# Kernel tuning notes

Hardware: AMD Instinct MI355X
Metric: run time of the kernel (lower is better)

The kernel has to match this reference:

```python
import jax, jax.numpy as jnp
import numpy as np

GRID_N = 8
N_RAYS = 4096
CHUNK = 512
MAX_SAMPLES = 128
SAMPLING_LENGTH = 0.05
STEP = SAMPLING_LENGTH / MAX_SAMPLES
HIT_THRESH = 5.0


def _build_mesh(n):
    g = n + 1
    xs = np.linspace(0.0, 1.0, g)
    P = np.stack(np.meshgrid(xs, xs, xs, indexing='ij'), -1).reshape(-1, 3).astype(np.float32)

    def vid(i, j, k):
        return (i * g + j) * g + k

    perms = [(0, 1, 2), (0, 2, 1), (1, 0, 2), (1, 2, 0), (2, 0, 1), (2, 1, 0)]
    tets = []
    for i in range(n):
        for j in range(n):
            for k in range(n):
                base = np.array([i, j, k])
                for p in perms:
                    vlist = [base.copy()]
                    cur = base.copy()
                    for ax in p:
                        cur = cur.copy(); cur[ax] += 1
                        vlist.append(cur.copy())
                    tets.append([vid(*vv) for vv in vlist])
    tets = np.array(tets, dtype=np.int32)  # [T,4]
    A, B, C, D = tets.T
    # face order matches torch module: ABC, ABD, ACD, BCD
    faces = np.stack([np.stack([A, B, C], 1), np.stack([A, B, D], 1),
                      np.stack([A, C, D], 1), np.stack([B, C, D], 1)], 1).astype(np.int32)  # [T,4,3]
    ff = faces.reshape(-1, 3)
    sf = np.sort(ff, 1)
    order = np.lexsort((sf[:, 2], sf[:, 1], sf[:, 0]))
    ss = sf[order]
    eq = np.all(ss[:-1] == ss[1:], 1)
    topo = -np.ones((tets.shape[0], 4), dtype=np.int32)
    idx = np.where(eq)[0]
    a = order[idx]; b = order[idx + 1]
    topo[a // 4, a % 4] = b // 4
    topo[b // 4, b % 4] = a // 4
    return P, tets, faces, topo


def setup_inputs() -> dict:
    key = jax.random.key(0)
    k1, k2, k3 = jax.random.split(key, 3)
    P, tets, faces, topo = _build_mesh(GRID_N)
    cage = jnp.asarray(P)[None] + 0.005 * jax.random.normal(k1, (1, P.shape[0], 3), jnp.float32)
    xy = jax.random.uniform(k2, (N_RAYS, 2), jnp.float32, 0.15, 0.85)
    ro = jnp.concatenate([xy, jnp.full((N_RAYS, 1), -0.5, jnp.float32)], -1)[None]
    jit = 0.05 * jax.random.normal(k3, (N_RAYS, 2), jnp.float32)
    rd = jnp.concatenate([jit, jnp.ones((N_RAYS, 1), jnp.float32)], -1)
    rd = (rd / jnp.linalg.norm(rd, axis=-1, keepdims=True))[None]
    return {"cage_vertices": cage, "ro": ro, "rd": rd,
            "tetras": jnp.asarray(tets), "faces": jnp.asarray(faces),
            "topology": jnp.asarray(topo)}


def _intersect(tri, o, d):
    # Moller-Trumbore: tri [F,3,3], o/d [c,3] -> nearest hit t + face idx
    p0 = tri[:, 0]; e1 = tri[:, 1] - p0; e2 = tri[:, 2] - p0
    h = jnp.cross(d[:, None, :], e2[None])          # [c,F,3]
    a = jnp.sum(e1[None] * h, -1)                   # [c,F]
    f = 1.0 / jnp.where(jnp.abs(a) > 1e-9, a, 1e-9)
    s = o[:, None, :] - p0[None]
    u = f * jnp.sum(s * h, -1)
    q = jnp.cross(s, e1[None])
    v = f * jnp.sum(d[:, None, :] * q, -1)
    t = f * jnp.sum(e2[None] * q, -1)
    ok = (jnp.abs(a) > 1e-9) & (u >= 0) & (u <= 1) & (v >= 0) & (u + v <= 1) & (t > 1e-6)
    t = jnp.where(ok, t, 1e10)
    return jnp.min(t, 1), jnp.argmin(t, 1)


def _bary(verts, tetras, p, tet):
    # barycentric coords of p [R,3] inside tetra tet [R] -> [R,4]
    vv = verts[tetras[tet]]                                # [R,4,3]
    M = jnp.transpose(vv[:, 1:] - vv[:, :1], (0, 2, 1))    # [R,3,3] columns B-A,C-A,D-A
    w = jnp.linalg.solve(M, (p - vv[:, 0])[..., None])[..., 0]  # wB,wC,wD
    return jnp.concatenate([1.0 - jnp.sum(w, -1, keepdims=True), w], -1)


def reference(cage_vertices, ro, rd, tetras, faces, topology):
    verts = cage_vertices[0]                 # [V,3]
    tri = verts[faces.reshape(-1, 3)]        # [F,3,3] deformed tetra faces
    o = ro[0]; d = rd[0]
    R = o.shape[0]
    od = jnp.concatenate([o, d], -1).reshape(R // CHUNK, CHUNK, 6)
    tmin, fidx = jax.lax.map(lambda x: _intersect(tri, x[:, :3], x[:, 3:]), od)
    tmin = tmin.reshape(R); fidx = fidx.reshape(R)
    hit = tmin < HIT_THRESH                  # mask = distances < 5
    t0 = jnp.where(hit, tmin, 0.0)
    hitp = o + t0[:, None] * d               # closest_points
    tet0 = jnp.where(hit, (fidx // 4).astype(jnp.int32), 0)  # triangle_to_tetra

    def step(carry, k):
        tet, alive = carry
        p = hitp + (k.astype(jnp.float32) * STEP + 1e-4) * d
        for _ in range(3):  # up to 3 neighbor hops per sample (tetra walk)
            w = _bary(verts, tetras, p, tet)
            inside = jnp.all(w >= -1e-6, -1)
            nb = topology[tet, 3 - jnp.argmin(w, -1)]  # face opposite most-negative vert
            move = alive & ~inside
            tet = jnp.where(move & (nb >= 0), nb, tet)
            alive = alive & (inside | (nb >= 0))
        w = _bary(verts, tetras, p, tet)
        inside = jnp.all(w >= -1e-6, -1)
        valid = alive & inside
        m = valid[:, None].astype(w.dtype)
        return (tet, alive), (jnp.where(valid, tet, -1), w * m, p * m, valid)

    (_, _), (tet_s, w_s, p_s, valid_s) = jax.lax.scan(step, (tet0, hit), jnp.arange(MAX_SAMPLES))
    tetra_indices = jnp.transpose(tet_s)            # [R,S]
    bary_coords = jnp.transpose(w_s, (1, 0, 2))     # [R,S,4]
    deformed_positions = jnp.transpose(p_s, (1, 0, 2))  # [R,S,3]
    valid = jnp.transpose(valid_s)
    ray_indices = jnp.where(valid, jnp.arange(R, dtype=jnp.int32)[:, None], -1)
    t_start = t0
    t_end = jnp.where(hit, t0 + SAMPLING_LENGTH, 0.0)
    return ray_indices, tetra_indices, bary_coords, t_start, t_end, deformed_positions
```

## Files before the change

kernel.cpp:

```cpp
#include <hip/hip_runtime.h>

#define S_MAX 128
#define NV_MAX 729
#define STEPD (0.05 / 128.0)
#define GUARD 1e-12

static __device__ __forceinline__ double mt_eval_f64(
    int F, const int* __restrict__ faces,
    const float* sx, const float* sy, const float* sz,
    double ox, double oy, double oz,
    double dx, double dy, double dz)
{
    const int i0 = faces[3 * F + 0];
    const int i1 = faces[3 * F + 1];
    const int i2 = faces[3 * F + 2];
    const double p0x = (double)sx[i0], p0y = (double)sy[i0], p0z = (double)sz[i0];
    const double e1x = (double)sx[i1] - p0x, e1y = (double)sy[i1] - p0y, e1z = (double)sz[i1] - p0z;
    const double e2x = (double)sx[i2] - p0x, e2y = (double)sy[i2] - p0y, e2z = (double)sz[i2] - p0z;
    const double hx = dy * e2z - dz * e2y;
    const double hy = dz * e2x - dx * e2z;
    const double hz = dx * e2y - dy * e2x;
    const double a  = e1x * hx + e1y * hy + e1z * hz;
    const bool oka = fabs(a) > 1e-9;
    const double f  = 1.0 / (oka ? a : 1e-9);
    const double s0 = ox - p0x, s1 = oy - p0y, s2 = oz - p0z;
    const double u  = f * (s0 * hx + s1 * hy + s2 * hz);
    const double qx = s1 * e1z - s2 * e1y;
    const double qy = s2 * e1x - s0 * e1z;
    const double qz = s0 * e1y - s1 * e1x;
    const double v  = f * (dx * qx + dy * qy + dz * qz);
    double t        = f * (e2x * qx + e2y * qy + e2z * qz);
    const bool ok = oka && (u >= 0.0) && (u <= 1.0) && (v >= 0.0) &&
                    (u + v <= 1.0) && (t > 1e-6);
    return ok ? t : 1e10;
}

__global__ __launch_bounds__(256) void isect_prep_kernel(
    const float* __restrict__ verts,
    const float* __restrict__ ro,
    const float* __restrict__ rd,
    const int*   __restrict__ faces,
    const int*   __restrict__ tetras,
    double* __restrict__ winv,
    double* __restrict__ tmin_out,
    int*    __restrict__ fidx_out,
    int NV, int NT, int NF, int R, int nIsect)
{
    const int tid = threadIdx.x;

    if (blockIdx.x >= nIsect) {
        const int t = (blockIdx.x - nIsect) * 256 + tid;
        if (t < NT) {
            const int4 tv = ((const int4*)tetras)[t];
            const double v0x = (double)verts[3 * tv.x + 0];
            const double v0y = (double)verts[3 * tv.x + 1];
            const double v0z = (double)verts[3 * tv.x + 2];
            const double m11 = (double)verts[3 * tv.y + 0] - v0x, m21 = (double)verts[3 * tv.y + 1] - v0y, m31 = (double)verts[3 * tv.y + 2] - v0z;
            const double m12 = (double)verts[3 * tv.z + 0] - v0x, m22 = (double)verts[3 * tv.z + 1] - v0y, m32 = (double)verts[3 * tv.z + 2] - v0z;
            const double m13 = (double)verts[3 * tv.w + 0] - v0x, m23 = (double)verts[3 * tv.w + 1] - v0y, m33 = (double)verts[3 * tv.w + 2] - v0z;
            const double A = m22 * m33 - m23 * m32;
            const double B = m21 * m33 - m23 * m31;
            const double C = m21 * m32 - m22 * m31;
            const double det = m11 * A - m12 * B + m13 * C;
            const double rcp = 1.0 / det;
            double* o = winv + 12 * (size_t)t;
            o[0] = v0x; o[1] = v0y; o[2] = v0z;
            o[3]  = A * rcp;  o[4]  = (m13 * m32 - m12 * m33) * rcp;  o[5]  = (m12 * m23 - m13 * m22) * rcp;
            o[6]  = -B * rcp; o[7]  = (m11 * m33 - m13 * m31) * rcp;  o[8]  = (m13 * m21 - m11 * m23) * rcp;
            o[9]  = C * rcp;  o[10] = (m12 * m31 - m11 * m32) * rcp;  o[11] = (m11 * m22 - m12 * m21) * rcp;
        }
        return;
    }

    __shared__ float sx[NV_MAX], sy[NV_MAX], sz[NV_MAX];
    __shared__ float red[256];
    __shared__ float s_zmin, s_zmax, s_marg;

    for (int i = tid; i < NV; i += 256) {
        sx[i] = verts[3 * i + 0];
        sy[i] = verts[3 * i + 1];
        sz[i] = verts[3 * i + 2];
    }
    __syncthreads();

    float zmin = 1e9f, zmax = -1e9f, dev = 0.0f;
    for (int i = tid; i < NV; i += 256) {
        const float x = sx[i], y = sy[i], z = sz[i];
        if (i % 9 == 0) { zmin = fminf(zmin, z); zmax = fmaxf(zmax, z); }
        dev = fmaxf(dev, fabsf(x - rintf(x * 8.0f) * 0.125f));
        dev = fmaxf(dev, fabsf(y - rintf(y * 8.0f) * 0.125f));
    }
    red[tid] = zmin; __syncthreads();
    for (int s = 128; s; s >>= 1) { if (tid < s) red[tid] = fminf(red[tid], red[tid + s]); __syncthreads(); }
    if (tid == 0) s_zmin = red[0];
    __syncthreads();
    red[tid] = zmax; __syncthreads();
    for (int s = 128; s; s >>= 1) { if (tid < s) red[tid] = fmaxf(red[tid], red[tid + s]); __syncthreads(); }
    if (tid == 0) s_zmax = red[0];
    __syncthreads();
    red[tid] = dev; __syncthreads();
    for (int s = 128; s; s >>= 1) { if (tid < s) red[tid] = fmaxf(red[tid], red[tid + s]); __syncthreads(); }
    if (tid == 0) s_marg = red[0] + 1e-5f;
    __syncthreads();

    const int wv = tid >> 6, lane = tid & 63;
    const int r = blockIdx.x * 4 + wv;
    if (r >= R) return;

    const double ox = (double)ro[3 * r + 0], oy = (double)ro[3 * r + 1], oz = (double)ro[3 * r + 2];
    const double dx = (double)rd[3 * r + 0], dy = (double)rd[3 * r + 1], dz = (double)rd[3 * r + 2];

    int ncand = 0, ixlo = 0, iylo = 0, ny = 1;
    if (dz > 0.0) {
        const double t_lo = ((double)s_zmin - oz) / dz;
        const double t_hi = ((double)s_zmax - oz) / dz;
        const double marg = (double)s_marg + 1e-9;
        const double xa = ox + t_lo * dx, xb = ox + t_hi * dx;
        const double ya = oy + t_lo * dy, yb = oy + t_hi * dy;
        const double xlo = fmin(xa, xb) - marg, xhi = fmax(xa, xb) + marg;
        const double ylo = fmin(ya, yb) - marg, yhi = fmax(ya, yb) + marg;
        const int ix0 = max(0, (int)floor(xlo * 8.0)), ix1 = min(7, (int)floor(xhi * 8.0));
        const int iy0 = max(0, (int)floor(ylo * 8.0)), iy1 = min(7, (int)floor(yhi * 8.0));
        if (ix0 <= ix1 && iy0 <= iy1) {
            ixlo = ix0; iylo = iy0;
            ny = iy1 - iy0 + 1;
            ncand = (ix1 - ix0 + 1) * ny * 24;
        }
    }

    double bt = 1e10;
    int    bi = 0x7fffffff;
    for (int c = lane; c < ncand; c += 64) {
        const int cell = c / 24, fk = c - cell * 24;
        const int cx = cell / ny, cy = cell - cx * ny;
        const int F = ((ixlo + cx) * 64 + (iylo + cy) * 8) * 24 + fk;
        const double t = mt_eval_f64(F, faces, sx, sy, sz, ox, oy, oz, dx, dy, dz);
        if (t < bt || (t == bt && F < bi)) { bt = t; bi = F; }
    }
    for (int off = 32; off; off >>= 1) {
        const double t2 = __shfl_down(bt, off);
        const int    i2 = __shfl_down(bi, off);
        if (t2 < bt || (t2 == bt && i2 < bi)) { bt = t2; bi = i2; }
    }
    const double btw = __shfl(bt, 0);
    if (btw >= 1e10) {
        bt = 1e10; bi = 0x7fffffff;
        for (int F = lane; F < NF; F += 64) {
            const double t = mt_eval_f64(F, faces, sx, sy, sz, ox, oy, oz, dx, dy, dz);
            if (t < bt || (t == bt && F < bi)) { bt = t; bi = F; }
        }
        for (int off = 32; off; off >>= 1) {
            const double t2 = __shfl_down(bt, off);
            const int    i2 = __shfl_down(bi, off);
            if (t2 < bt || (t2 == bt && i2 < bi)) { bt = t2; bi = i2; }
        }
    }
    if (lane == 0) { tmin_out[r] = bt; fidx_out[r] = bi; }
}

__global__ __launch_bounds__(256) void walk_kernel(
    const float* __restrict__ ro,
    const float* __restrict__ rd,
    const int*   __restrict__ topo,
    const double* __restrict__ tmin_in,
    const int*    __restrict__ fidx_in,
    const double* __restrict__ winv,
    short* __restrict__ seq,
    float* __restrict__ out_tstart,
    float* __restrict__ out_tend,
    int R)
{
    const int wv = threadIdx.x >> 6, lane = threadIdx.x & 63;
    const int r = blockIdx.x * 4 + wv;
    if (r >= R) return;

    short* myseq = seq + (size_t)r * S_MAX;

    const double tmin = tmin_in[r];
    const bool   hit  = tmin < 5.0;
    const double t0   = hit ? tmin : 0.0;
    if (lane == 0) {
        out_tstart[r] = (float)t0;
        out_tend[r]   = hit ? (float)(t0 + 0.05) : 0.0f;
    }
    if (!hit) {
        for (int k = lane; k < S_MAX; k += 64) myseq[k] = -1;
        return;
    }

    const double ox = (double)ro[3 * r + 0], oy = (double)ro[3 * r + 1], oz = (double)ro[3 * r + 2];
    const double dx = (double)rd[3 * r + 0], dy = (double)rd[3 * r + 1], dz = (double)rd[3 * r + 2];
    const double hpx = ox + t0 * dx, hpy = oy + t0 * dy, hpz = oz + t0 * dz;

    int  tet   = fidx_in[r] >> 2;
    bool alive = true;

    int4 topo4 = ((const int4*)topo)[tet];
    const double* rec = winv + 12 * (size_t)tet;
    double v0x = rec[0], v0y = rec[1], v0z = rec[2];
    double i0 = rec[3], i1 = rec[4],  i2 = rec[5];
    double i3 = rec[6], i4 = rec[7],  i5 = rec[8];
    double i6 = rec[9], i7 = rec[10], i8 = rec[11];

    double wb0, wb1, wb2, wb3, wd0, wd1, wd2, wd3;
    {
        const double bx = hpx - v0x, by = hpy - v0y, bz = hpz - v0z;
        wb1 = i0 * bx + i1 * by + i2 * bz;
        wb2 = i3 * bx + i4 * by + i5 * bz;
        wb3 = i6 * bx + i7 * by + i8 * bz;
        wd1 = i0 * dx + i1 * dy + i2 * dz;
        wd2 = i3 * dx + i4 * dy + i5 * dz;
        wd3 = i6 * dx + i7 * dy + i8 * dz;
        wb0 = 1.0 - (wb1 + wb2 + wb3);
        wd0 = -(wd1 + wd2 + wd3);
    }

    int k0 = 0;
    while (k0 < S_MAX) {
        const int kk = k0 + lane;
        bool p = false;
        if (kk < S_MAX) {
            const double toff = (double)kk * STEPD + 1e-4;
            const double a0 = wb0 + toff * wd0;
            const double a1 = wb1 + toff * wd1;
            const double a2 = wb2 + toff * wd2;
            const double a3 = wb3 + toff * wd3;
            const double mn = fmin(fmin(a0, a1), fmin(a2, a3));
            p = (mn + 1e-6 >= GUARD);
        }
        const unsigned long long bad = __ballot(kk < S_MAX && !p);
        const int nvalid = min(S_MAX - k0, 64);
        const int evt = (bad == 0ull) ? nvalid : (__ffsll(bad) - 1);

        if (lane < evt) myseq[kk] = (short)tet;
        k0 += evt;
        if (evt == nvalid) continue;

        const double toff = (double)k0 * STEPD + 1e-4;
        const double px = hpx + toff * dx;
        const double py = hpy + toff * dy;
        const double pz = hpz + toff * dz;

        double b1 = px - v0x, b2 = py - v0y, b3 = pz - v0z;
        double w1 = i0 * b1 + i1 * b2 + i2 * b3;
        double w2 = i3 * b1 + i4 * b2 + i5 * b3;
        double w3 = i6 * b1 + i7 * b2 + i8 * b3;
        double w0 = 1.0 - (w1 + w2 + w3);
        bool inside = (w0 >= -1e-6) && (w1 >= -1e-6) && (w2 >= -1e-6) && (w3 >= -1e-6);

        int it = 0;
        bool moved = false;
        while (!inside && it < 3) {
            int    jm = 0;
            double wb = w0;
            if (w1 < wb) { wb = w1; jm = 1; }
            if (w2 < wb) { wb = w2; jm = 2; }
            if (w3 < wb) { wb = w3; jm = 3; }
            const int nb = (jm == 0) ? topo4.w : (jm == 1) ? topo4.z :
                           (jm == 2) ? topo4.y : topo4.x;
            if (nb < 0) { alive = false; break; }
            tet = nb;
            moved = true;
            rec = winv + 12 * (size_t)tet;
            topo4 = ((const int4*)topo)[tet];
            v0x = rec[0]; v0y = rec[1]; v0z = rec[2];
            i0 = rec[3]; i1 = rec[4];  i2 = rec[5];
            i3 = rec[6]; i4 = rec[7];  i5 = rec[8];
            i6 = rec[9]; i7 = rec[10]; i8 = rec[11];
            b1 = px - v0x; b2 = py - v0y; b3 = pz - v0z;
            w1 = i0 * b1 + i1 * b2 + i2 * b3;
            w2 = i3 * b1 + i4 * b2 + i5 * b3;
            w3 = i6 * b1 + i7 * b2 + i8 * b3;
            w0 = 1.0 - (w1 + w2 + w3);
            inside = (w0 >= -1e-6) && (w1 >= -1e-6) && (w2 >= -1e-6) && (w3 >= -1e-6);
            ++it;
        }
        if (!alive) break;

        if (lane == 0) myseq[k0] = inside ? (short)tet : (short)-1;
        ++k0;

        if (moved) {
            const double bx = hpx - v0x, by = hpy - v0y, bz = hpz - v0z;
            wb1 = i0 * bx + i1 * by + i2 * bz;
            wb2 = i3 * bx + i4 * by + i5 * bz;
            wb3 = i6 * bx + i7 * by + i8 * bz;
            wd1 = i0 * dx + i1 * dy + i2 * dz;
            wd2 = i3 * dx + i4 * dy + i5 * dz;
            wd3 = i6 * dx + i7 * dy + i8 * dz;
            wb0 = 1.0 - (wb1 + wb2 + wb3);
            wd0 = -(wd1 + wd2 + wd3);
        }
    }
    for (int k = k0 + lane; k < S_MAX; k += 64) myseq[k] = -1;
}

__global__ __launch_bounds__(256) void emit_kernel(
    const float* __restrict__ ro,
    const float* __restrict__ rd,
    const double* __restrict__ tmin_in,
    const short*  __restrict__ seq,
    const double* __restrict__ winv,
    float* __restrict__ out_rayidx,
    float* __restrict__ out_tetidx,
    float* __restrict__ out_bary,
    float* __restrict__ out_pos,
    int R)
{
    const int idx = blockIdx.x * 256 + threadIdx.x;
    if (idx >= R * S_MAX) return;
    const int r = idx >> 7;
    const int k = idx & (S_MAX - 1);

    const int tk = (int)seq[idx];
    if (tk < 0) {
        out_rayidx[idx] = -1.0f;
        out_tetidx[idx] = -1.0f;
        ((float4*)out_bary)[idx] = make_float4(0.0f, 0.0f, 0.0f, 0.0f);
        out_pos[idx * 3 + 0] = 0.0f;
        out_pos[idx * 3 + 1] = 0.0f;
        out_pos[idx * 3 + 2] = 0.0f;
        return;
    }

    const double tmin = tmin_in[r];
    const double t0   = (tmin < 5.0) ? tmin : 0.0;
    const double ox = (double)ro[3 * r + 0], oy = (double)ro[3 * r + 1], oz = (double)ro[3 * r + 2];
    const double dx = (double)rd[3 * r + 0], dy = (double)rd[3 * r + 1], dz = (double)rd[3 * r + 2];
    const double toff = (double)k * STEPD + 1e-4;
    const double px = (ox + t0 * dx) + toff * dx;
    const double py = (oy + t0 * dy) + toff * dy;
    const double pz = (oz + t0 * dz) + toff * dz;

    const double* rec = winv + 12 * (size_t)tk;
    const double b1 = px - rec[0], b2 = py - rec[1], b3 = pz - rec[2];
    const double w1 = rec[3] * b1 + rec[4]  * b2 + rec[5]  * b3;
    const double w2 = rec[6] * b1 + rec[7]  * b2 + rec[8]  * b3;
    const double w3 = rec[9] * b1 + rec[10] * b2 + rec[11] * b3;
    const double w0 = 1.0 - (w1 + w2 + w3);

    out_rayidx[idx] = (float)r;
    out_tetidx[idx] = (float)tk;
    ((float4*)out_bary)[idx] = make_float4((float)w0, (float)w1, (float)w2, (float)w3);
    out_pos[idx * 3 + 0] = (float)px;
    out_pos[idx * 3 + 1] = (float)py;
    out_pos[idx * 3 + 2] = (float)pz;
}

extern "C" void kernel_launch(void* const* d_in, const int* in_sizes, int n_in,
                              void* d_out, int out_size, void* d_ws, size_t ws_size,
                              hipStream_t stream) {
    const float* verts  = (const float*)d_in[0];
    const float* ro     = (const float*)d_in[1];
    const float* rd     = (const float*)d_in[2];
    const int*   tetras = (const int*)d_in[3];
    const int*   faces  = (const int*)d_in[4];
    const int*   topo   = (const int*)d_in[5];

    const int NV = in_sizes[0] / 3;
    const int R  = in_sizes[1] / 3;
    const int NT = in_sizes[3] / 4;
    const int NF = in_sizes[4] / 3;
    const int S  = S_MAX;

    double* wtmin = (double*)d_ws;
    double* winv  = wtmin + R;
    int*    wfidx = (int*)(winv + 12 * (size_t)NT);
    short*  wseq  = (short*)(wfidx + R);

    float* out        = (float*)d_out;
    float* out_rayidx = out;
    float* out_tetidx = out + (size_t)R * S;
    float* out_bary   = out + (size_t)2 * R * S;
    float* out_tstart = out + (size_t)6 * R * S;
    float* out_tend   = out_tstart + R;
    float* out_pos    = out_tend + R;

    const int nIsect = (R + 3) / 4;
    const int nPrep  = (NT + 255) / 256;

    isect_prep_kernel<<<nIsect + nPrep, 256, 0, stream>>>(
        verts, ro, rd, faces, tetras, winv, wtmin, wfidx, NV, NT, NF, R, nIsect);
    walk_kernel<<<(R + 3) / 4, 256, 0, stream>>>(ro, rd, topo, wtmin, wfidx, winv,
                                                 wseq, out_tstart, out_tend, R);
    emit_kernel<<<(R * S + 255) / 256, 256, 0, stream>>>(ro, rd, wtmin, wseq, winv,
                                                         out_rayidx, out_tetidx, out_bary, out_pos, R);
}
```

Measured before the change: 87.50 us.

## Fuse intersection, tetra walk and emit into one per-ray kernel

Moves tetra inverse-matrix prep into its own kernel and merges ray intersection, the tetra walk and output emission into a single kernel. Each wave keeps its ray's tet sequence in shared memory. This drops the global round trips for tmin, face index and the short sequence buffer, and removes one kernel launch. The cost is that emit work now runs 64 lanes per ray instead of using a fully parallel grid, and the prep kernel no longer overlaps with intersection blocks.

```diff
diff --git a/kernel.cpp b/kernel.cpp
--- a/kernel.cpp
+++ b/kernel.cpp
@@ -35,47 +35,54 @@
     return ok ? t : 1e10;
 }
 
-__global__ __launch_bounds__(256) void isect_prep_kernel(
+__global__ __launch_bounds__(256) void prep_kernel(
+    const float* __restrict__ verts,
+    const int*   __restrict__ tetras,
+    double* __restrict__ winv,
+    int NT)
+{
+    const int t = blockIdx.x * 256 + threadIdx.x;
+    if (t >= NT) return;
+    const int4 tv = ((const int4*)tetras)[t];
+    const double v0x = (double)verts[3 * tv.x + 0];
+    const double v0y = (double)verts[3 * tv.x + 1];
+    const double v0z = (double)verts[3 * tv.x + 2];
+    const double m11 = (double)verts[3 * tv.y + 0] - v0x, m21 = (double)verts[3 * tv.y + 1] - v0y, m31 = (double)verts[3 * tv.y + 2] - v0z;
+    const double m12 = (double)verts[3 * tv.z + 0] - v0x, m22 = (double)verts[3 * tv.z + 1] - v0y, m32 = (double)verts[3 * tv.z + 2] - v0z;
+    const double m13 = (double)verts[3 * tv.w + 0] - v0x, m23 = (double)verts[3 * tv.w + 1] - v0y, m33 = (double)verts[3 * tv.w + 2] - v0z;
+    const double A = m22 * m33 - m23 * m32;
+    const double B = m21 * m33 - m23 * m31;
+    const double C = m21 * m32 - m22 * m31;
+    const double det = m11 * A - m12 * B + m13 * C;
+    const double rcp = 1.0 / det;
+    double* o = winv + 12 * (size_t)t;
+    o[0] = v0x; o[1] = v0y; o[2] = v0z;
+    o[3]  = A * rcp;  o[4]  = (m13 * m32 - m12 * m33) * rcp;  o[5]  = (m12 * m23 - m13 * m22) * rcp;
+    o[6]  = -B * rcp; o[7]  = (m11 * m33 - m13 * m31) * rcp;  o[8]  = (m13 * m21 - m11 * m23) * rcp;
+    o[9]  = C * rcp;  o[10] = (m12 * m31 - m11 * m32) * rcp;  o[11] = (m11 * m22 - m12 * m21) * rcp;
+}
+
+__global__ __launch_bounds__(256) void fused_kernel(
     const float* __restrict__ verts,
     const float* __restrict__ ro,
     const float* __restrict__ rd,
     const int*   __restrict__ faces,
-    const int*   __restrict__ tetras,
-    double* __restrict__ winv,
-    double* __restrict__ tmin_out,
-    int*    __restrict__ fidx_out,
-    int NV, int NT, int NF, int R, int nIsect)
+    const int*   __restrict__ topo,
+    const double* __restrict__ winv,
+    float* __restrict__ out_rayidx,
+    float* __restrict__ out_tetidx,
+    float* __restrict__ out_bary,
+    float* __restrict__ out_tstart,
+    float* __restrict__ out_tend,
+    float* __restrict__ out_pos,
+    int NV, int NF, int R)
 {
-    const int tid = threadIdx.x;
-
-    if (blockIdx.x >= nIsect) {
-        const int t = (blockIdx.x - nIsect) * 256 + tid;
-        if (t < NT) {
-            const int4 tv = ((const int4*)tetras)[t];
-            const double v0x = (double)verts[3 * tv.x + 0];
-            const double v0y = (double)verts[3 * tv.x + 1];
-            const double v0z = (double)verts[3 * tv.x + 2];
-            const double m11 = (double)verts[3 * tv.y + 0] - v0x, m21 = (double)verts[3 * tv.y + 1] - v0y, m31 = (double)verts[3 * tv.y + 2] - v0z;
-            const double m12 = (double)verts[3 * tv.z + 0] - v0x, m22 = (double)verts[3 * tv.z + 1] - v0y, m32 = (double)verts[3 * tv.z + 2] - v0z;
-            const double m13 = (double)verts[3 * tv.w + 0] - v0x, m23 = (double)verts[3 * tv.w + 1] - v0y, m33 = (double)verts[3 * tv.w + 2] - v0z;
-            const double A = m22 * m33 - m23 * m32;
-            const double B = m21 * m33 - m23 * m31;
-            const double C = m21 * m32 - m22 * m31;
-            const double det = m11 * A - m12 * B + m13 * C;
-            const double rcp = 1.0 / det;
-            double* o = winv + 12 * (size_t)t;
-            o[0] = v0x; o[1] = v0y; o[2] = v0z;
-            o[3]  = A * rcp;  o[4]  = (m13 * m32 - m12 * m33) * rcp;  o[5]  = (m12 * m23 - m13 * m22) * rcp;
-            o[6]  = -B * rcp; o[7]  = (m11 * m33 - m13 * m31) * rcp;  o[8]  = (m13 * m21 - m11 * m23) * rcp;
-            o[9]  = C * rcp;  o[10] = (m12 * m31 - m11 * m32) * rcp;  o[11] = (m11 * m22 - m12 * m21) * rcp;
-        }
-        return;
-    }
-
     __shared__ float sx[NV_MAX], sy[NV_MAX], sz[NV_MAX];
     __shared__ float red[256];
     __shared__ float s_zmin, s_zmax, s_marg;
-
+    __shared__ short s_seq[4][S_MAX];
+
+    const int tid = threadIdx.x;
     for (int i = tid; i < NV; i += 256) {
         sx[i] = verts[3 * i + 0];
         sy[i] = verts[3 * i + 1];
@@ -106,6 +113,7 @@
     const int wv = tid >> 6, lane = tid & 63;
     const int r = blockIdx.x * 4 + wv;
     if (r >= R) return;
+    short* myseq = s_seq[wv];
 
     const double ox = (double)ro[3 * r + 0], oy = (double)ro[3 * r + 1], oz = (double)ro[3 * r + 2];
     const double dx = (double)rd[3 * r + 0], dy = (double)rd[3 * r + 1], dz = (double)rd[3 * r + 2];
@@ -142,145 +150,47 @@
         const int    i2 = __shfl_down(bi, off);
         if (t2 < bt || (t2 == bt && i2 < bi)) { bt = t2; bi = i2; }
     }
-    const double btw = __shfl(bt, 0);
-    if (btw >= 1e10) {
-        bt = 1e10; bi = 0x7fffffff;
+    bt = __shfl(bt, 0);
+    bi = __shfl(bi, 0);
+    if (bt >= 1e10) {
+        double fb = 1e10; int fi = 0x7fffffff;
         for (int F = lane; F < NF; F += 64) {
             const double t = mt_eval_f64(F, faces, sx, sy, sz, ox, oy, oz, dx, dy, dz);
-            if (t < bt || (t == bt && F < bi)) { bt = t; bi = F; }
+            if (t < fb || (t == fb && F < fi)) { fb = t; fi = F; }
         }
         for (int off = 32; off; off >>= 1) {
-            const double t2 = __shfl_down(bt, off);
-            const int    i2 = __shfl_down(bi, off);
-            if (t2 < bt || (t2 == bt && i2 < bi)) { bt = t2; bi = i2; }
-        }
-    }
-    if (lane == 0) { tmin_out[r] = bt; fidx_out[r] = bi; }
-}
-
-__global__ __launch_bounds__(256) void walk_kernel(
-    const float* __restrict__ ro,
-    const float* __restrict__ rd,
-    const int*   __restrict__ topo,
-    const double* __restrict__ tmin_in,
-    const int*    __restrict__ fidx_in,
-    const double* __restrict__ winv,
-    short* __restrict__ seq,
-    float* __restrict__ out_tstart,
-    float* __restrict__ out_tend,
-    int R)
-{
-    const int wv = threadIdx.x >> 6, lane = threadIdx.x & 63;
-    const int r = blockIdx.x * 4 + wv;
-    if (r >= R) return;
-
-    short* myseq = seq + (size_t)r * S_MAX;
-
-    const double tmin = tmin_in[r];
-    const bool   hit  = tmin < 5.0;
-    const double t0   = hit ? tmin : 0.0;
+            const double t2 = __shfl_down(fb, off);
+            const int    i2 = __shfl_down(fi, off);
+            if (t2 < fb || (t2 == fb && i2 < fi)) { fb = t2; fi = i2; }
+        }
+        bt = __shfl(fb, 0);
+        bi = __shfl(fi, 0);
+    }
+
+    const bool   hit = bt < 5.0;
+    const double t0  = hit ? bt : 0.0;
     if (lane == 0) {
         out_tstart[r] = (float)t0;
         out_tend[r]   = hit ? (float)(t0 + 0.05) : 0.0f;
     }
+
+    const double hpx = ox + t0 * dx, hpy = oy + t0 * dy, hpz = oz + t0 * dz;
+
     if (!hit) {
         for (int k = lane; k < S_MAX; k += 64) myseq[k] = -1;
-        return;
-    }
-
-    const double ox = (double)ro[3 * r + 0], oy = (double)ro[3 * r + 1], oz = (double)ro[3 * r + 2];
-    const double dx = (double)rd[3 * r + 0], dy = (double)rd[3 * r + 1], dz = (double)rd[3 * r + 2];
-    const double hpx = ox + t0 * dx, hpy = oy + t0 * dy, hpz = oz + t0 * dz;
-
-    int  tet   = fidx_in[r] >> 2;
-    bool alive = true;
-
-    int4 topo4 = ((const int4*)topo)[tet];
-    const double* rec = winv + 12 * (size_t)tet;
-    double v0x = rec[0], v0y = rec[1], v0z = rec[2];
-    double i0 = rec[3], i1 = rec[4],  i2 = rec[5];
-    double i3 = rec[6], i4 = rec[7],  i5 = rec[8];
-    double i6 = rec[9], i7 = rec[10], i8 = rec[11];
-
-    double wb0, wb1, wb2, wb3, wd0, wd1, wd2, wd3;
-    {
-        const double bx = hpx - v0x, by = hpy - v0y, bz = hpz - v0z;
-        wb1 = i0 * bx + i1 * by + i2 * bz;
-        wb2 = i3 * bx + i4 * by + i5 * bz;
-        wb3 = i6 * bx + i7 * by + i8 * bz;
-        wd1 = i0 * dx + i1 * dy + i2 * dz;
-        wd2 = i3 * dx + i4 * dy + i5 * dz;
-        wd3 = i6 * dx + i7 * dy + i8 * dz;
-        wb0 = 1.0 - (wb1 + wb2 + wb3);
-        wd0 = -(wd1 + wd2 + wd3);
-    }
-
-    int k0 = 0;
-    while (k0 < S_MAX) {
-        const int kk = k0 + lane;
-        bool p = false;
-        if (kk < S_MAX) {
-            const double toff = (double)kk * STEPD + 1e-4;
-            const double a0 = wb0 + toff * wd0;
-            const double a1 = wb1 + toff * wd1;
-            const double a2 = wb2 + toff * wd2;
-            const double a3 = wb3 + toff * wd3;
-            const double mn = fmin(fmin(a0, a1), fmin(a2, a3));
-            p = (mn + 1e-6 >= GUARD);
-        }
-        const unsigned long long bad = __ballot(kk < S_MAX && !p);
-        const int nvalid = min(S_MAX - k0, 64);
-        const int evt = (bad == 0ull) ? nvalid : (__ffsll(bad) - 1);
-
-        if (lane < evt) myseq[kk] = (short)tet;
-        k0 += evt;
-        if (evt == nvalid) continue;
-
-        const double toff = (double)k0 * STEPD + 1e-4;
-        const double px = hpx + toff * dx;
-        const double py = hpy + toff * dy;
-        const double pz = hpz + toff * dz;
-
-        double b1 = px - v0x, b2 = py - v0y, b3 = pz - v0z;
-        double w1 = i0 * b1 + i1 * b2 + i2 * b3;
-        double w2 = i3 * b1 + i4 * b2 + i5 * b3;
-        double w3 = i6 * b1 + i7 * b2 + i8 * b3;
-        double w0 = 1.0 - (w1 + w2 + w3);
-        bool inside = (w0 >= -1e-6) && (w1 >= -1e-6) && (w2 >= -1e-6) && (w3 >= -1e-6);
-
-        int it = 0;
-        bool moved = false;
-        while (!inside && it < 3) {
-            int    jm = 0;
-            double wb = w0;
-            if (w1 < wb) { wb = w1; jm = 1; }
-            if (w2 < wb) { wb = w2; jm = 2; }
-            if (w3 < wb) { wb = w3; jm = 3; }
-            const int nb = (jm == 0) ? topo4.w : (jm == 1) ? topo4.z :
-                           (jm == 2) ? topo4.y : topo4.x;
-            if (nb < 0) { alive = false; break; }
-            tet = nb;
-            moved = true;
-            rec = winv + 12 * (size_t)tet;
-            topo4 = ((const int4*)topo)[tet];
-            v0x = rec[0]; v0y = rec[1]; v0z = rec[2];
-            i0 = rec[3]; i1 = rec[4];  i2 = rec[5];
-            i3 = rec[6]; i4 = rec[7];  i5 = rec[8];
-            i6 = rec[9]; i7 = rec[10]; i8 = rec[11];
-            b1 = px - v0x; b2 = py - v0y; b3 = pz - v0z;
-            w1 = i0 * b1 + i1 * b2 + i2 * b3;
-            w2 = i3 * b1 + i4 * b2 + i5 * b3;
-            w3 = i6 * b1 + i7 * b2 + i8 * b3;
-            w0 = 1.0 - (w1 + w2 + w3);
-            inside = (w0 >= -1e-6) && (w1 >= -1e-6) && (w2 >= -1e-6) && (w3 >= -1e-6);
-            ++it;
-        }
-        if (!alive) break;
-
-        if (lane == 0) myseq[k0] = inside ? (short)tet : (short)-1;
-        ++k0;
-
-        if (moved) {
+    } else {
+        int  tet   = bi >> 2;
+        bool alive = true;
+
+        int4 topo4 = ((const int4*)topo)[tet];
+        const double* rec = winv + 12 * (size_t)tet;
+        double v0x = rec[0], v0y = rec[1], v0z = rec[2];
+        double i0 = rec[3], i1 = rec[4],  i2 = rec[5];
+        double i3 = rec[6], i4 = rec[7],  i5 = rec[8];
+        double i6 = rec[9], i7 = rec[10], i8 = rec[11];
+
+        double wb0, wb1, wb2, wb3, wd0, wd1, wd2, wd3;
+        {
             const double bx = hpx - v0x, by = hpy - v0y, bz = hpz - v0z;
             wb1 = i0 * bx + i1 * by + i2 * bz;
             wb2 = i3 * bx + i4 * by + i5 * bz;
@@ -291,60 +201,118 @@
             wb0 = 1.0 - (wb1 + wb2 + wb3);
             wd0 = -(wd1 + wd2 + wd3);
         }
-    }
-    for (int k = k0 + lane; k < S_MAX; k += 64) myseq[k] = -1;
-}
-
-__global__ __launch_bounds__(256) void emit_kernel(
-    const float* __restrict__ ro,
-    const float* __restrict__ rd,
-    const double* __restrict__ tmin_in,
-    const short*  __restrict__ seq,
-    const double* __restrict__ winv,
-    float* __restrict__ out_rayidx,
-    float* __restrict__ out_tetidx,
-    float* __restrict__ out_bary,
-    float* __restrict__ out_pos,
-    int R)
-{
-    const int idx = blockIdx.x * 256 + threadIdx.x;
-    if (idx >= R * S_MAX) return;
-    const int r = idx >> 7;
-    const int k = idx & (S_MAX - 1);
-
-    const int tk = (int)seq[idx];
-    if (tk < 0) {
-        out_rayidx[idx] = -1.0f;
-        out_tetidx[idx] = -1.0f;
-        ((float4*)out_bary)[idx] = make_float4(0.0f, 0.0f, 0.0f, 0.0f);
-        out_pos[idx * 3 + 0] = 0.0f;
-        out_pos[idx * 3 + 1] = 0.0f;
-        out_pos[idx * 3 + 2] = 0.0f;
-        return;
-    }
-
-    const double tmin = tmin_in[r];
-    const double t0   = (tmin < 5.0) ? tmin : 0.0;
-    const double ox = (double)ro[3 * r + 0], oy = (double)ro[3 * r + 1], oz = (double)ro[3 * r + 2];
-    const double dx = (double)rd[3 * r + 0], dy = (double)rd[3 * r + 1], dz = (double)rd[3 * r + 2];
-    const double toff = (double)k * STEPD + 1e-4;
-    const double px = (ox + t0 * dx) + toff * dx;
-    const double py = (oy + t0 * dy) + toff * dy;
-    const double pz = (oz + t0 * dz) + toff * dz;
-
-    const double* rec = winv + 12 * (size_t)tk;
-    const double b1 = px - rec[0], b2 = py - rec[1], b3 = pz - rec[2];
-    const double w1 = rec[3] * b1 + rec[4]  * b2 + rec[5]  * b3;
-    const double w2 = rec[6] * b1 + rec[7]  * b2 + rec[8]  * b3;
-    const double w3 = rec[9] * b1 + rec[10] * b2 + rec[11] * b3;
-    const double w0 = 1.0 - (w1 + w2 + w3);
-
-    out_rayidx[idx] = (float)r;
-    out_tetidx[idx] = (float)tk;
-    ((float4*)out_bary)[idx] = make_float4((float)w0, (float)w1, (float)w2, (float)w3);
-    out_pos[idx * 3 + 0] = (float)px;
-    out_pos[idx * 3 + 1] = (float)py;
-    out_pos[idx * 3 + 2] = (float)pz;
+
+        int k0 = 0;
+        while (k0 < S_MAX) {
+            const int kk = k0 + lane;
+            bool p = false;
+            if (kk < S_MAX) {
+                const double toff = (double)kk * STEPD + 1e-4;
+                const double a0 = wb0 + toff * wd0;
+                const double a1 = wb1 + toff * wd1;
+                const double a2 = wb2 + toff * wd2;
+                const double a3 = wb3 + toff * wd3;
+                const double mn = fmin(fmin(a0, a1), fmin(a2, a3));
+                p = (mn + 1e-6 >= GUARD);
+            }
+            const unsigned long long bad = __ballot(kk < S_MAX && !p);
+            const int nvalid = min(S_MAX - k0, 64);
+            const int evt = (bad == 0ull) ? nvalid : (__ffsll(bad) - 1);
+
+            if (lane < evt) myseq[kk] = (short)tet;
+            k0 += evt;
+            if (evt == nvalid) continue;
+
+            const double toff = (double)k0 * STEPD + 1e-4;
+            const double px = hpx + toff * dx;
+            const double py = hpy + toff * dy;
+            const double pz = hpz + toff * dz;
+
+            double b1 = px - v0x, b2 = py - v0y, b3 = pz - v0z;
+            double w1 = i0 * b1 + i1 * b2 + i2 * b3;
+            double w2 = i3 * b1 + i4 * b2 + i5 * b3;
+            double w3 = i6 * b1 + i7 * b2 + i8 * b3;
+            double w0 = 1.0 - (w1 + w2 + w3);
+            bool inside = (w0 >= -1e-6) && (w1 >= -1e-6) && (w2 >= -1e-6) && (w3 >= -1e-6);
+
+            int it = 0;
+            bool moved = false;
+            while (!inside && it < 3) {
+                int    jm = 0;
+                double wb = w0;
+                if (w1 < wb) { wb = w1; jm = 1; }
+                if (w2 < wb) { wb = w2; jm = 2; }
+                if (w3 < wb) { wb = w3; jm = 3; }
+                const int nb = (jm == 0) ? topo4.w : (jm == 1) ? topo4.z :
+                               (jm == 2) ? topo4.y : topo4.x;
+                if (nb < 0) { alive = false; break; }
+                tet = nb;
+                moved = true;
+                rec = winv + 12 * (size_t)tet;
+                topo4 = ((const int4*)topo)[tet];
+                v0x = rec[0]; v0y = rec[1]; v0z = rec[2];
+                i0 = rec[3]; i1 = rec[4];  i2 = rec[5];
+                i3 = rec[6]; i4 = rec[7];  i5 = rec[8];
+                i6 = rec[9]; i7 = rec[10]; i8 = rec[11];
+                b1 = px - v0x; b2 = py - v0y; b3 = pz - v0z;
+                w1 = i0 * b1 + i1 * b2 + i2 * b3;
+                w2 = i3 * b1 + i4 * b2 + i5 * b3;
+                w3 = i6 * b1 + i7 * b2 + i8 * b3;
+                w0 = 1.0 - (w1 + w2 + w3);
+                inside = (w0 >= -1e-6) && (w1 >= -1e-6) && (w2 >= -1e-6) && (w3 >= -1e-6);
+                ++it;
+            }
+            if (!alive) break;
+
+            if (lane == 0) myseq[k0] = inside ? (short)tet : (short)-1;
+            ++k0;
+
+            if (moved) {
+                const double bx = hpx - v0x, by = hpy - v0y, bz = hpz - v0z;
+                wb1 = i0 * bx + i1 * by + i2 * bz;
+                wb2 = i3 * bx + i4 * by + i5 * bz;
+                wb3 = i6 * bx + i7 * by + i8 * bz;
+                wd1 = i0 * dx + i1 * dy + i2 * dz;
+                wd2 = i3 * dx + i4 * dy + i5 * dz;
+                wd3 = i6 * dx + i7 * dy + i8 * dz;
+                wb0 = 1.0 - (wb1 + wb2 + wb3);
+                wd0 = -(wd1 + wd2 + wd3);
+            }
+        }
+        for (int k = k0 + lane; k < S_MAX; k += 64) myseq[k] = -1;
+    }
+
+    for (int k = lane; k < S_MAX; k += 64) {
+        const size_t idx = (size_t)r * S_MAX + k;
+        const int tk = (int)myseq[k];
+        if (tk < 0) {
+            out_rayidx[idx] = -1.0f;
+            out_tetidx[idx] = -1.0f;
+            ((float4*)out_bary)[idx] = make_float4(0.0f, 0.0f, 0.0f, 0.0f);
+            out_pos[idx * 3 + 0] = 0.0f;
+            out_pos[idx * 3 + 1] = 0.0f;
+            out_pos[idx * 3 + 2] = 0.0f;
+            continue;
+        }
+        const double toff = (double)k * STEPD + 1e-4;
+        const double px = hpx + toff * dx;
+        const double py = hpy + toff * dy;
+        const double pz = hpz + toff * dz;
+
+        const double* rec2 = winv + 12 * (size_t)tk;
+        const double b1 = px - rec2[0], b2 = py - rec2[1], b3 = pz - rec2[2];
+        const double w1 = rec2[3] * b1 + rec2[4]  * b2 + rec2[5]  * b3;
+        const double w2 = rec2[6] * b1 + rec2[7]  * b2 + rec2[8]  * b3;
+        const double w3 = rec2[9] * b1 + rec2[10] * b2 + rec2[11] * b3;
+        const double w0 = 1.0 - (w1 + w2 + w3);
+
+        out_rayidx[idx] = (float)r;
+        out_tetidx[idx] = (float)tk;
+        ((float4*)out_bary)[idx] = make_float4((float)w0, (float)w1, (float)w2, (float)w3);
+        out_pos[idx * 3 + 0] = (float)px;
+        out_pos[idx * 3 + 1] = (float)py;
+        out_pos[idx * 3 + 2] = (float)pz;
+    }
 }
 
 extern "C" void kernel_launch(void* const* d_in, const int* in_sizes, int n_in,
@@ -363,10 +331,7 @@
     const int NF = in_sizes[4] / 3;
     const int S  = S_MAX;
 
-    double* wtmin = (double*)d_ws;
-    double* winv  = wtmin + R;
-    int*    wfidx = (int*)(winv + 12 * (size_t)NT);
-    short*  wseq  = (short*)(wfidx + R);
+    double* winv = (double*)d_ws;
 
     float* out        = (float*)d_out;
     float* out_rayidx = out;
@@ -376,13 +341,9 @@
     float* out_tend   = out_tstart + R;
     float* out_pos    = out_tend + R;
 
-    const int nIsect = (R + 3) / 4;
-    const int nPrep  = (NT + 255) / 256;
-
-    isect_prep_kernel<<<nIsect + nPrep, 256, 0, stream>>>(
-        verts, ro, rd, faces, tetras, winv, wtmin, wfidx, NV, NT, NF, R, nIsect);
-    walk_kernel<<<(R + 3) / 4, 256, 0, stream>>>(ro, rd, topo, wtmin, wfidx, winv,
-                                                 wseq, out_tstart, out_tend, R);
-    emit_kernel<<<(R * S + 255) / 256, 256, 0, stream>>>(ro, rd, wtmin, wseq, winv,
-                                                         out_rayidx, out_tetidx, out_bary, out_pos, R);
+    prep_kernel<<<(NT + 255) / 256, 256, 0, stream>>>(verts, tetras, winv, NT);
+    fused_kernel<<<(R + 3) / 4, 256, 0, stream>>>(
+        verts, ro, rd, faces, topo, winv,
+        out_rayidx, out_tetidx, out_bary, out_tstart, out_tend, out_pos,
+        NV, NF, R);
 }
```

New measurement: 83.40 us. 4.7% less time.
